# Kernel tuning notes

Hardware: AMD Instinct MI355X
Metric: run time of the kernel (lower is better)

The kernel has to match this reference:

```python
import jax, jax.numpy as jnp
import numpy as np

NHEAD = 8

def setup_inputs() -> dict:
    key = jax.random.key(0)
    ks = jax.random.split(key, 6)
    b, n, d = 4, 1024, 512
    emb = jax.random.normal(ks[0], (b, n, d), dtype=jnp.float32)
    dirs = jax.random.normal(ks[1], (b, n, n, 3), dtype=jnp.float32)
    d_mask = jax.random.normal(ks[2], (b * NHEAD, n, n), dtype=jnp.float32) * 0.1
    W_proj = jax.random.normal(ks[3], (d, 3 * d), dtype=jnp.float32) / np.sqrt(d)
    b_proj = jnp.zeros((3 * d,), dtype=jnp.float32)
    w_force = jax.random.normal(ks[4], (d,), dtype=jnp.float32) / np.sqrt(d)
    b_force = jnp.zeros((1,), dtype=jnp.float32)
    return {"emb": emb, "dirs": dirs, "d_mask": d_mask, "W_proj": W_proj,
            "b_proj": b_proj, "w_force": w_force, "b_force": b_force}

def reference(emb, dirs, d_mask, W_proj, b_proj, w_force, b_force):
    b, n, d = emb.shape
    h = NHEAD
    dh = d // h
    scale = jnp.asarray(np.sqrt(d), emb.dtype)
    qkv = emb @ W_proj + b_proj                      # (b,n,3d)
    q, k, v = jnp.split(qkv, 3, axis=-1)
    q = q.reshape(b, n, h, dh).transpose(0, 2, 1, 3) / scale   # (b,h,n,dh)
    k = k.reshape(b, n, h, dh).transpose(0, 2, 1, 3)           # (b,h,n,dh)
    v = v.reshape(b, n, h, dh).transpose(0, 2, 1, 3)           # (b,h,n,dh)
    scores = jnp.einsum('bhid,bhjd->bhij', q, k) + d_mask.reshape(b, h, n, n)
    attn = jax.nn.softmax(scores, axis=-1)                     # (b,h,n,n); dropout in eval mode = identity
    # torch: (attn[...,None] * dirs[:,None]) @ v  materializes (b,h,n,n,3);
    # fused einsum computes the same per-axis weighted sum without it.
    xyz = jnp.einsum('bhij,bija,bhjd->biahd', attn, dirs, v)   # (b,n,3,h,dh)
    xyz = xyz.reshape(b, n, 3, d)
    out = jnp.einsum('bnad,d->bna', xyz, w_force) + b_force[0]  # (b,n,3)
    return out
```

## Files before the change

kernel.cpp:

```cpp
#include <hip/hip_runtime.h>
#include <hip/hip_bf16.h>

#define NH 8
#define BB 4
#define NN 1024
#define DD 512
#define DH 64
#define SCS 1032

typedef __bf16 bf16x8 __attribute__((ext_vector_type(8)));
typedef float f32x4 __attribute__((ext_vector_type(4)));

__device__ __forceinline__ unsigned short f2bf(float f) {
    union { float f; unsigned u; } v; v.f = f;
    unsigned u = v.u;
    unsigned r = u + 0x7FFFu + ((u >> 16) & 1u);
    return (unsigned short)(r >> 16);
}
__device__ __forceinline__ float b2f(unsigned short u) {
    union { unsigned u; float f; } cv; cv.u = ((unsigned)u) << 16; return cv.f;
}

__global__ __launch_bounds__(256) void k_prep(const float* __restrict__ W,
                                              const float* __restrict__ b_proj,
                                              const float* __restrict__ w_force,
                                              unsigned short* __restrict__ Wt,
                                              float* __restrict__ bias_eff,
                                              float* __restrict__ wv_eff,
                                              float* __restrict__ s_bias) {
    __shared__ float tile[32][33];
    int bx = blockIdx.x;
    int t = threadIdx.x;
    const float rscale = 0.044194173824159216f;
    if (bx < 512) {
        int c0 = (bx & 15) * 32;
        int n0 = (bx >> 4) * 32;
        for (int i = 0; i < 4; ++i) {
            int idx = t + i * 256;
            int r = idx >> 5, cn = idx & 31;
            tile[r][cn] = W[(c0 + r) * (3 * DD) + n0 + cn];
        }
        __syncthreads();
        for (int i = 0; i < 4; ++i) {
            int idx = t + i * 256;
            int nn = idx >> 5, cc = idx & 31;
            float v = tile[cc][nn];
            int n = n0 + nn;
            if (n < DD) v *= rscale;
            Wt[n * DD + c0 + cc] = f2bf(v);
        }
        if ((bx & 15) == 0 && t < 32) {
            int n = n0 + t;
            bias_eff[n] = b_proj[n] * (n < DD ? rscale : 1.0f);
        }
        return;
    }
    int wave = t >> 6, lane = t & 63;
    if (bx == 640) {
        if (wave == 0) {
            for (int hh = 0; hh < NH; ++hh) {
                float p = b_proj[2 * DD + hh * DH + lane] * w_force[hh * DH + lane];
                for (int off = 32; off; off >>= 1) p += __shfl_xor(p, off);
                if (lane == 0) s_bias[hh] = p;
            }
        }
        return;
    }
    int c = (bx - 512) * 4 + wave;
    const float* wr = W + (size_t)c * (3 * DD) + 2 * DD;
    #pragma unroll
    for (int hh = 0; hh < NH; ++hh) {
        float p = wr[hh * DH + lane] * w_force[hh * DH + lane];
        for (int off = 32; off; off >>= 1) p += __shfl_xor(p, off);
        if (lane == 0) wv_eff[c * 8 + hh] = p;
    }
}

__global__ __launch_bounds__(128) void k_s(const float* __restrict__ emb,
                                           const float* __restrict__ wv_eff,
                                           const float* __restrict__ s_bias,
                                           float* __restrict__ s_ws) {
    int t = blockIdx.x * 128 + threadIdx.x;
    int row = t >> 3;
    int h = t & 7;
    const float* er = emb + (size_t)row * DD;
    const float* wp = wv_eff + h;
    float acc = 0.f;
    #pragma unroll 8
    for (int c4 = 0; c4 < DD / 4; ++c4) {
        float4 e = *(const float4*)(er + c4 * 4);
        acc += e.x * wp[(c4 * 4 + 0) * 8];
        acc += e.y * wp[(c4 * 4 + 1) * 8];
        acc += e.z * wp[(c4 * 4 + 2) * 8];
        acc += e.w * wp[(c4 * 4 + 3) * 8];
    }
    int b = row >> 10, j = row & 1023;
    s_ws[(b * 8 + h) * NN + j] = acc + s_bias[h];
}

__global__ __launch_bounds__(256) void k_gemm(const float* __restrict__ emb,
                                              const unsigned short* __restrict__ Wt,
                                              const float* __restrict__ bias_eff,
                                              unsigned short* __restrict__ qb,
                                              unsigned short* __restrict__ kb) {
    __shared__ __align__(16) unsigned short a_s[128 * 32];
    __shared__ __align__(16) unsigned short b_s[128 * 32];
    int m0 = blockIdx.x * 128, n0 = blockIdx.y * 128;
    int t = threadIdx.x;
    int wave = t >> 6, lane = t & 63;
    int wr = (wave >> 1) * 64, wc = (wave & 1) * 64;
    int qd = lane >> 4, c = lane & 15;
    int sr = t >> 2, sg = (t & 3) * 8;
    f32x4 acc[4][4] = {};
    for (int k0 = 0; k0 < DD; k0 += 32) {
        float4 x0 = *(const float4*)(emb + (size_t)(m0 + sr) * DD + k0 + sg);
        float4 x1 = *(const float4*)(emb + (size_t)(m0 + sr) * DD + k0 + sg + 4);
        float4 y0 = *(const float4*)(emb + (size_t)(m0 + 64 + sr) * DD + k0 + sg);
        float4 y1 = *(const float4*)(emb + (size_t)(m0 + 64 + sr) * DD + k0 + sg + 4);
        uint4 bv0 = *(const uint4*)(Wt + (size_t)(n0 + sr) * DD + k0 + sg);
        uint4 bv1 = *(const uint4*)(Wt + (size_t)(n0 + 64 + sr) * DD + k0 + sg);
        union { unsigned short u[8]; uint4 v; } px, py;
        px.u[0] = f2bf(x0.x); px.u[1] = f2bf(x0.y); px.u[2] = f2bf(x0.z); px.u[3] = f2bf(x0.w);
        px.u[4] = f2bf(x1.x); px.u[5] = f2bf(x1.y); px.u[6] = f2bf(x1.z); px.u[7] = f2bf(x1.w);
        py.u[0] = f2bf(y0.x); py.u[1] = f2bf(y0.y); py.u[2] = f2bf(y0.z); py.u[3] = f2bf(y0.w);
        py.u[4] = f2bf(y1.x); py.u[5] = f2bf(y1.y); py.u[6] = f2bf(y1.z); py.u[7] = f2bf(y1.w);
        __syncthreads();
        *(uint4*)(&a_s[sr * 32 + sg]) = px.v;
        *(uint4*)(&a_s[(64 + sr) * 32 + sg]) = py.v;
        *(uint4*)(&b_s[sr * 32 + sg]) = bv0;
        *(uint4*)(&b_s[(64 + sr) * 32 + sg]) = bv1;
        __syncthreads();
        bf16x8 af[4], bfr[4];
        #pragma unroll
        for (int mi = 0; mi < 4; ++mi)
            af[mi] = *(const bf16x8*)(&a_s[(wr + mi * 16 + c) * 32 + qd * 8]);
        #pragma unroll
        for (int ni = 0; ni < 4; ++ni)
            bfr[ni] = *(const bf16x8*)(&b_s[(wc + ni * 16 + c) * 32 + qd * 8]);
        #pragma unroll
        for (int mi = 0; mi < 4; ++mi)
            #pragma unroll
            for (int ni = 0; ni < 4; ++ni)
                acc[mi][ni] = __builtin_amdgcn_mfma_f32_16x16x32_bf16(af[mi], bfr[ni], acc[mi][ni], 0, 0, 0);
    }
    bool isQ = (n0 < DD);
    unsigned short* dst = isQ ? qb : kb;
    int nb = isQ ? n0 : n0 - DD;
    #pragma unroll
    for (int mi = 0; mi < 4; ++mi)
        #pragma unroll
        for (int ni = 0; ni < 4; ++ni) {
            int col = nb + wc + ni * 16 + c;
            float be = bias_eff[isQ ? col : col + DD];
            #pragma unroll
            for (int r = 0; r < 4; ++r) {
                int row = m0 + wr + mi * 16 + qd * 4 + r;
                dst[(size_t)row * DD + col] = f2bf(acc[mi][ni][r] + be);
            }
        }
}

__global__ __launch_bounds__(256) void k_attn(const unsigned short* __restrict__ qb,
                                              const unsigned short* __restrict__ kb,
                                              const float* __restrict__ s_ws,
                                              const float* __restrict__ d_mask,
                                              const float* __restrict__ dirs,
                                              float* __restrict__ part) {
    __shared__ unsigned short sc_s[16 * SCS];
    int blk = blockIdx.x;
    int itile = blk & 63;
    int bh = blk >> 6;
    int h = bh & 7;
    int b = bh >> 3;
    int i0 = itile * 16;
    int t = threadIdx.x;
    int w = t >> 6, lane = t & 63, qd = lane >> 4, c = lane & 15;

    const unsigned short* qbase = qb + ((size_t)(b * NN + i0 + c) * DD + h * DH + qd * 8);
    bf16x8 aq0 = *(const bf16x8*)(qbase);
    bf16x8 aq1 = *(const bf16x8*)(qbase + 32);
    int j0w = w * 256;
    #pragma unroll
    for (int jt = 0; jt < 16; ++jt) {
        int j0 = j0w + jt * 16;
        const unsigned short* kba = kb + ((size_t)(b * NN + j0 + c) * DD + h * DH + qd * 8);
        bf16x8 kf0 = *(const bf16x8*)(kba);
        bf16x8 kf1 = *(const bf16x8*)(kba + 32);
        f32x4 sc = {0.f, 0.f, 0.f, 0.f};
        sc = __builtin_amdgcn_mfma_f32_16x16x32_bf16(kf0, aq0, sc, 0, 0, 0);
        sc = __builtin_amdgcn_mfma_f32_16x16x32_bf16(kf1, aq1, sc, 0, 0, 0);
        ushort4 pk;
        pk.x = f2bf(sc[0]); pk.y = f2bf(sc[1]); pk.z = f2bf(sc[2]); pk.w = f2bf(sc[3]);
        *(ushort4*)(&sc_s[c * SCS + j0 + qd * 4]) = pk;
    }
    __syncthreads();

    const float* sm = s_ws + bh * NN;
    float4 sv[4];
    #pragma unroll
    for (int seg = 0; seg < 4; ++seg)
        sv[seg] = *(const float4*)(sm + seg * 256 + lane * 4);

    const float* mbase = d_mask + (size_t)bh * NN * NN;
    const float* dbase = dirs + (size_t)b * NN * NN * 3;

    #pragma unroll
    for (int r4 = 0; r4 < 4; ++r4) {
        int il = w * 4 + r4;
        int i = i0 + il;
        const float* mrow = mbase + (size_t)i * NN + lane * 4;
        const float* drow = dbase + ((size_t)i * NN + lane * 4) * 3;
        float l = 0.f, a0 = 0.f, a1 = 0.f, a2 = 0.f;
        #pragma unroll
        for (int seg = 0; seg < 4; ++seg) {
            float4 mk = *(const float4*)(mrow + seg * 256);
            float4 d0 = *(const float4*)(drow + seg * 768);
            float4 d1 = *(const float4*)(drow + seg * 768 + 4);
            float4 d2 = *(const float4*)(drow + seg * 768 + 8);
            ushort4 scv = *(const ushort4*)(&sc_s[il * SCS + seg * 256 + lane * 4]);
            float p0 = __expf(b2f(scv.x) + mk.x);
            float p1 = __expf(b2f(scv.y) + mk.y);
            float p2 = __expf(b2f(scv.z) + mk.z);
            float p3 = __expf(b2f(scv.w) + mk.w);
            l += p0 + p1 + p2 + p3;
            float t0 = p0 * sv[seg].x, t1 = p1 * sv[seg].y;
            float t2 = p2 * sv[seg].z, t3 = p3 * sv[seg].w;
            a0 += t0 * d0.x + t1 * d0.w + t2 * d1.z + t3 * d2.y;
            a1 += t0 * d0.y + t1 * d1.x + t2 * d1.w + t3 * d2.z;
            a2 += t0 * d0.z + t1 * d1.y + t2 * d2.x + t3 * d2.w;
        }
        #pragma unroll
        for (int off = 1; off < 64; off <<= 1) {
            l  += __shfl_xor(l, off);
            a0 += __shfl_xor(a0, off);
            a1 += __shfl_xor(a1, off);
            a2 += __shfl_xor(a2, off);
        }
        if (lane == 0) {
            f32x4 o; o[0] = l; o[1] = a0; o[2] = a1; o[3] = a2;
            *(f32x4*)(part + ((size_t)bh * NN + i) * 4) = o;
        }
    }
}

__global__ __launch_bounds__(256) void k_fin(const float4* __restrict__ part,
                                             const float* __restrict__ b_force,
                                             float* __restrict__ out) {
    int t = blockIdx.x * 256 + threadIdx.x;
    int b = t >> 10, i = t & 1023;
    float o0, o1, o2;
    o0 = o1 = o2 = b_force[0];
    #pragma unroll
    for (int h = 0; h < NH; ++h) {
        float4 p = part[(((size_t)(b * NH + h)) << 10) + i];
        float inv = 1.0f / p.x;
        o0 += p.y * inv; o1 += p.z * inv; o2 += p.w * inv;
    }
    out[t * 3 + 0] = o0;
    out[t * 3 + 1] = o1;
    out[t * 3 + 2] = o2;
}

extern "C" void kernel_launch(void* const* d_in, const int* in_sizes, int n_in,
                              void* d_out, int out_size, void* d_ws, size_t ws_size,
                              hipStream_t stream) {
    (void)in_sizes; (void)n_in; (void)out_size; (void)ws_size;
    const float* emb     = (const float*)d_in[0];
    const float* dirs    = (const float*)d_in[1];
    const float* d_mask  = (const float*)d_in[2];
    const float* W       = (const float*)d_in[3];
    const float* b_proj  = (const float*)d_in[4];
    const float* w_force = (const float*)d_in[5];
    const float* b_force = (const float*)d_in[6];
    float* out = (float*)d_out;

    char* ws = (char*)d_ws;
    float* wv_eff   = (float*)ws;
    float* s_bias   = wv_eff + 4096;
    float* bias_eff = s_bias + 8;
    float* s_ws     = bias_eff + 1024;
    unsigned short* Wt = (unsigned short*)(s_ws + 32768);
    unsigned short* qb = Wt + 1024 * 512;
    unsigned short* kb = qb + 4096 * 512;
    float* part = (float*)(kb + 4096 * 512);

    hipLaunchKernelGGL(k_prep, dim3(641),      dim3(256), 0, stream,
                       W, b_proj, w_force, Wt, bias_eff, wv_eff, s_bias);
    hipLaunchKernelGGL(k_s,    dim3(256),      dim3(128), 0, stream, emb, wv_eff, s_bias, s_ws);
    hipLaunchKernelGGL(k_gemm, dim3(32, 8),    dim3(256), 0, stream, emb, Wt, bias_eff, qb, kb);
    hipLaunchKernelGGL(k_attn, dim3(BB * NH * 64), dim3(256), 0, stream,
                       qb, kb, s_ws, d_mask, dirs, part);
    hipLaunchKernelGGL(k_fin,  dim3(16),       dim3(256), 0, stream, (const float4*)part, b_force, out);
}
```

Baseline: 313.6 us.

## Process all heads per block so dirs rows are loaded once

The attention kernel now assigns one block per batch and 8-row tile, with each of its 8 waves computing QK scores for one head. The softmax-weighted reduction then loops over all heads per row, so each dirs row is read once instead of once per head, which cuts a large global read volume. In exchange the 16-row MFMA tile carries only 8 useful rows, so half the score compute is wasted. It also needs about 132KB of shared memory per block and holds many per-head accumulators in registers, which limits occupancy.

```diff
diff --git a/kernel.cpp b/kernel.cpp
--- a/kernel.cpp
+++ b/kernel.cpp
@@ -160,85 +160,93 @@
         }
 }
 
-__global__ __launch_bounds__(256) void k_attn(const unsigned short* __restrict__ qb,
-                                              const unsigned short* __restrict__ kb,
-                                              const float* __restrict__ s_ws,
-                                              const float* __restrict__ d_mask,
-                                              const float* __restrict__ dirs,
-                                              float* __restrict__ part) {
-    __shared__ unsigned short sc_s[16 * SCS];
+__global__ __launch_bounds__(512, 2) void k_attn(const unsigned short* __restrict__ qb,
+                                                 const unsigned short* __restrict__ kb,
+                                                 const float* __restrict__ s_ws,
+                                                 const float* __restrict__ d_mask,
+                                                 const float* __restrict__ dirs,
+                                                 float* __restrict__ part) {
+    __shared__ unsigned short sc_s[NH * 8 * SCS];
     int blk = blockIdx.x;
-    int itile = blk & 63;
-    int bh = blk >> 6;
-    int h = bh & 7;
-    int b = bh >> 3;
-    int i0 = itile * 16;
+    int b = blk >> 7;
+    int itile = blk & 127;
+    int i0 = itile * 8;
     int t = threadIdx.x;
     int w = t >> 6, lane = t & 63, qd = lane >> 4, c = lane & 15;
 
-    const unsigned short* qbase = qb + ((size_t)(b * NN + i0 + c) * DD + h * DH + qd * 8);
-    bf16x8 aq0 = *(const bf16x8*)(qbase);
-    bf16x8 aq1 = *(const bf16x8*)(qbase + 32);
-    int j0w = w * 256;
-    #pragma unroll
-    for (int jt = 0; jt < 16; ++jt) {
-        int j0 = j0w + jt * 16;
-        const unsigned short* kba = kb + ((size_t)(b * NN + j0 + c) * DD + h * DH + qd * 8);
-        bf16x8 kf0 = *(const bf16x8*)(kba);
-        bf16x8 kf1 = *(const bf16x8*)(kba + 32);
-        f32x4 sc = {0.f, 0.f, 0.f, 0.f};
-        sc = __builtin_amdgcn_mfma_f32_16x16x32_bf16(kf0, aq0, sc, 0, 0, 0);
-        sc = __builtin_amdgcn_mfma_f32_16x16x32_bf16(kf1, aq1, sc, 0, 0, 0);
-        ushort4 pk;
-        pk.x = f2bf(sc[0]); pk.y = f2bf(sc[1]); pk.z = f2bf(sc[2]); pk.w = f2bf(sc[3]);
-        *(ushort4*)(&sc_s[c * SCS + j0 + qd * 4]) = pk;
+    {
+        int h = w;
+        const unsigned short* qbase =
+            qb + ((size_t)(b * NN + i0 + (c & 7)) * DD + h * DH + qd * 8);
+        bf16x8 aq0 = *(const bf16x8*)(qbase);
+        bf16x8 aq1 = *(const bf16x8*)(qbase + 32);
+        #pragma unroll 8
+        for (int jt = 0; jt < 64; ++jt) {
+            int j0 = jt * 16;
+            const unsigned short* kba =
+                kb + ((size_t)(b * NN + j0 + c) * DD + h * DH + qd * 8);
+            bf16x8 kf0 = *(const bf16x8*)(kba);
+            bf16x8 kf1 = *(const bf16x8*)(kba + 32);
+            f32x4 sc = {0.f, 0.f, 0.f, 0.f};
+            sc = __builtin_amdgcn_mfma_f32_16x16x32_bf16(kf0, aq0, sc, 0, 0, 0);
+            sc = __builtin_amdgcn_mfma_f32_16x16x32_bf16(kf1, aq1, sc, 0, 0, 0);
+            ushort4 pk;
+            pk.x = f2bf(sc[0]); pk.y = f2bf(sc[1]); pk.z = f2bf(sc[2]); pk.w = f2bf(sc[3]);
+            if (c < 8)
+                *(ushort4*)(&sc_s[(h * 8 + c) * SCS + j0 + qd * 4]) = pk;
+        }
     }
     __syncthreads();
 
-    const float* sm = s_ws + bh * NN;
-    float4 sv[4];
-    #pragma unroll
-    for (int seg = 0; seg < 4; ++seg)
-        sv[seg] = *(const float4*)(sm + seg * 256 + lane * 4);
-
-    const float* mbase = d_mask + (size_t)bh * NN * NN;
-    const float* dbase = dirs + (size_t)b * NN * NN * 3;
-
-    #pragma unroll
-    for (int r4 = 0; r4 < 4; ++r4) {
-        int il = w * 4 + r4;
-        int i = i0 + il;
-        const float* mrow = mbase + (size_t)i * NN + lane * 4;
-        const float* drow = dbase + ((size_t)i * NN + lane * 4) * 3;
-        float l = 0.f, a0 = 0.f, a1 = 0.f, a2 = 0.f;
-        #pragma unroll
-        for (int seg = 0; seg < 4; ++seg) {
-            float4 mk = *(const float4*)(mrow + seg * 256);
-            float4 d0 = *(const float4*)(drow + seg * 768);
-            float4 d1 = *(const float4*)(drow + seg * 768 + 4);
-            float4 d2 = *(const float4*)(drow + seg * 768 + 8);
-            ushort4 scv = *(const ushort4*)(&sc_s[il * SCS + seg * 256 + lane * 4]);
-            float p0 = __expf(b2f(scv.x) + mk.x);
-            float p1 = __expf(b2f(scv.y) + mk.y);
-            float p2 = __expf(b2f(scv.z) + mk.z);
-            float p3 = __expf(b2f(scv.w) + mk.w);
-            l += p0 + p1 + p2 + p3;
-            float t0 = p0 * sv[seg].x, t1 = p1 * sv[seg].y;
-            float t2 = p2 * sv[seg].z, t3 = p3 * sv[seg].w;
-            a0 += t0 * d0.x + t1 * d0.w + t2 * d1.z + t3 * d2.y;
-            a1 += t0 * d0.y + t1 * d1.x + t2 * d1.w + t3 * d2.z;
-            a2 += t0 * d0.z + t1 * d1.y + t2 * d2.x + t3 * d2.w;
-        }
+    int il = w;
+    int i = i0 + il;
+    const float* drb = dirs + ((size_t)b * NN * NN + (size_t)i * NN + lane * 4) * 3;
+    const float* mbb = d_mask + ((size_t)(b * NH) * NN + i) * NN + lane * 4;
+    const float* svb = s_ws + (size_t)(b * NH) * NN + lane * 4;
+
+    float l[NH] = {}, A0[NH] = {}, A1[NH] = {}, A2[NH] = {};
+    #pragma unroll
+    for (int seg = 0; seg < 4; ++seg) {
+        const float* dr = drb + seg * 768;
+        float4 d0 = *(const float4*)(dr);
+        float4 d1 = *(const float4*)(dr + 4);
+        float4 d2 = *(const float4*)(dr + 8);
+        float4 mk[NH], sv[NH];
+        ushort4 scv[NH];
+        #pragma unroll
+        for (int h = 0; h < NH; ++h) {
+            mk[h] = *(const float4*)(mbb + (size_t)h * NN * NN + seg * 256);
+            sv[h] = *(const float4*)(svb + h * NN + seg * 256);
+            scv[h] = *(const ushort4*)(&sc_s[(h * 8 + il) * SCS + seg * 256 + lane * 4]);
+        }
+        #pragma unroll
+        for (int h = 0; h < NH; ++h) {
+            float p0 = __expf(b2f(scv[h].x) + mk[h].x);
+            float p1 = __expf(b2f(scv[h].y) + mk[h].y);
+            float p2 = __expf(b2f(scv[h].z) + mk[h].z);
+            float p3 = __expf(b2f(scv[h].w) + mk[h].w);
+            l[h] += p0 + p1 + p2 + p3;
+            float t0 = p0 * sv[h].x, t1 = p1 * sv[h].y;
+            float t2 = p2 * sv[h].z, t3 = p3 * sv[h].w;
+            A0[h] += t0 * d0.x + t1 * d0.w + t2 * d1.z + t3 * d2.y;
+            A1[h] += t0 * d0.y + t1 * d1.x + t2 * d1.w + t3 * d2.z;
+            A2[h] += t0 * d0.z + t1 * d1.y + t2 * d2.x + t3 * d2.w;
+        }
+    }
+
+    #pragma unroll
+    for (int h = 0; h < NH; ++h) {
+        float L = l[h], x = A0[h], y = A1[h], z = A2[h];
         #pragma unroll
         for (int off = 1; off < 64; off <<= 1) {
-            l  += __shfl_xor(l, off);
-            a0 += __shfl_xor(a0, off);
-            a1 += __shfl_xor(a1, off);
-            a2 += __shfl_xor(a2, off);
+            L += __shfl_xor(L, off);
+            x += __shfl_xor(x, off);
+            y += __shfl_xor(y, off);
+            z += __shfl_xor(z, off);
         }
         if (lane == 0) {
-            f32x4 o; o[0] = l; o[1] = a0; o[2] = a1; o[3] = a2;
-            *(f32x4*)(part + ((size_t)bh * NN + i) * 4) = o;
+            f32x4 o; o[0] = L; o[1] = x; o[2] = y; o[3] = z;
+            *(f32x4*)(part + ((size_t)(b * NH + h) * NN + i) * 4) = o;
         }
     }
 }
@@ -288,7 +296,7 @@
                        W, b_proj, w_force, Wt, bias_eff, wv_eff, s_bias);
     hipLaunchKernelGGL(k_s,    dim3(256),      dim3(128), 0, stream, emb, wv_eff, s_bias, s_ws);
     hipLaunchKernelGGL(k_gemm, dim3(32, 8),    dim3(256), 0, stream, emb, Wt, bias_eff, qb, kb);
-    hipLaunchKernelGGL(k_attn, dim3(BB * NH * 64), dim3(256), 0, stream,
+    hipLaunchKernelGGL(k_attn, dim3(BB * 128), dim3(512), 0, stream,
                        qb, kb, s_ws, d_mask, dirs, part);
     hipLaunchKernelGGL(k_fin,  dim3(16),       dim3(256), 0, stream, (const float4*)part, b_force, out);
 }
```

After: 383.1 us. +22.2%, slower.
